# Kernel optimization log

Hardware: AMD Instinct MI355X
Metric: run time of the kernel (lower is better)

## Reference

```python
import jax, jax.numpy as jnp
import numpy as np


def setup_inputs() -> dict:
    key = jax.random.key(0)
    k1, k2, k3 = jax.random.split(key, 3)
    B, S, D_IN, D_OUT = 8, 512, 4096, 16384
    x = jax.random.normal(k1, (B, S, D_IN), dtype=jnp.float32)
    # int8 weights stored as int32 values in [-128, 127] (int8 semantics)
    weight_int8 = jax.random.randint(k2, (D_OUT, D_IN), -128, 128, dtype=jnp.int32)
    # per-tensor scale, e.g. max_abs/127 of an fp32 weight with std ~0.02
    weight_scale = jnp.float32(0.02 * 4.0 / 127.0)
    bias = jax.random.normal(k3, (D_OUT,), dtype=jnp.float32) * 0.01
    return {"x": x, "weight_int8": weight_int8, "weight_scale": weight_scale, "bias": bias}


def reference(x, weight_int8, weight_scale, bias):
    # dequantize: materialize fp32 weight (per-tensor scale, zero_point = 0)
    weight_fp32 = weight_int8.astype(jnp.float32) * weight_scale  # [O, I]
    # F.linear: y = x @ W^T + b
    out = jnp.einsum("bsi,oi->bso", x, weight_fp32) + bias
    return out
```

## Files before the change

### kernel.cpp

```cpp
#include <hip/hip_runtime.h>
#include <stdint.h>
#include <stddef.h>

typedef __attribute__((ext_vector_type(4))) int       i32x4;
typedef __attribute__((ext_vector_type(8))) short     bf16x8;
typedef __attribute__((ext_vector_type(4))) float     f32x4;
typedef __attribute__((ext_vector_type(4))) float     f32x4v;
typedef __attribute__((ext_vector_type(4))) unsigned short u16x4;

__device__ __forceinline__ unsigned short f2bf(float f) {
    union { float f; unsigned u; } v; v.f = f;
    unsigned r = v.u + 0x7FFFu + ((v.u >> 16) & 1u);
    return (unsigned short)(r >> 16);
}

__device__ __forceinline__ void gload_lds16(const void* g, void* l) {
    __builtin_amdgcn_global_load_lds(
        (const __attribute__((address_space(1))) void*)(g),
        (__attribute__((address_space(3))) void*)(l), 16, 0, 0);
}

__device__ __forceinline__ int pack4(float a, float b, float c, float d, float inv) {
    int r0 = ((int)rintf(a * inv)) & 255;
    int r1 = ((int)rintf(b * inv)) & 255;
    int r2 = ((int)rintf(c * inv)) & 255;
    int r3 = ((int)rintf(d * inv)) & 255;
    return r0 | (r1 << 8) | (r2 << 16) | (r3 << 24);
}

__global__ void cvt_x_q8(const float* __restrict__ x, signed char* __restrict__ xq,
                         float* __restrict__ sx, int K) {
    const int row = blockIdx.x;
    const int t   = threadIdx.x;
    const float* xr = x + (size_t)row * K;
    const int ng = K / 1024;

    f32x4v v[8];
    float am = 0.f;
#pragma unroll
    for (int i = 0; i < 8; ++i) {
        if (i < ng) {
            v[i] = ((const f32x4v*)xr)[i * 256 + t];
            am = fmaxf(am, fmaxf(fmaxf(fabsf(v[i][0]), fabsf(v[i][1])),
                                 fmaxf(fabsf(v[i][2]), fabsf(v[i][3]))));
        }
    }
#pragma unroll
    for (int m = 32; m >= 1; m >>= 1) am = fmaxf(am, __shfl_xor(am, m, 64));
    __shared__ float red[4];
    const int w = t >> 6;
    if ((t & 63) == 0) red[w] = am;
    __syncthreads();
    am = fmaxf(fmaxf(red[0], red[1]), fmaxf(red[2], red[3]));

    const float inv = (am > 0.f) ? 127.0f / am : 0.f;
    if (t == 0) sx[row] = (am > 0.f) ? am / 127.0f : 0.f;

    int* oq = (int*)(xq + (size_t)row * K);
#pragma unroll
    for (int i = 0; i < 8; ++i)
        if (i < ng) oq[i * 256 + t] = pack4(v[i][0], v[i][1], v[i][2], v[i][3], inv);
}

__global__ void cvt_w_q8(const int* __restrict__ w, signed char* __restrict__ o, int n4) {
    int i = blockIdx.x * blockDim.x + threadIdx.x;
    int stride = gridDim.x * blockDim.x;
    for (; i < n4; i += stride) {
        i32x4 a = ((const i32x4*)w)[i];
        ((int*)o)[i] = (a[0] & 255) | ((a[1] & 255) << 8) | ((a[2] & 255) << 16) | ((a[3] & 255) << 24);
    }
}

#define BM8 256
#define BN8 256
#define BKQ 128

__global__ __launch_bounds__(512, 2) void gemm8p_i8(
    const signed char* __restrict__ A,
    const signed char* __restrict__ Bw,
    const float* __restrict__ sx,
    const float* __restrict__ scale_p,
    const float* __restrict__ bias,
    float* __restrict__ C,
    int M, int N, int K)
{
    __shared__ __align__(16) char smem[131072];

    const int t    = threadIdx.x;
    const int lane = t & 63;
    const int w    = t >> 6;
    const int wm   = w >> 2;
    const int wn   = w & 3;

    int nwg = gridDim.x, bid = blockIdx.x;
    int swz = ((nwg & 7) == 0) ? ((bid & 7) * (nwg >> 3) + (bid >> 3)) : bid;
    const int ntn  = N / BN8;
    const int row0 = (swz / ntn) * BM8;
    const int col0 = (swz % ntn) * BN8;

    const int Kb = K;
    const int NT = K / BKQ;

    const int srow = w * 8 + (lane >> 3);
    const int sc2  = ((lane & 7) ^ (lane >> 3)) * 16;
    const int ldsLaneOff = w * 1024 + lane * 16;

    const char* aG = (const char*)A + (size_t)(row0 + srow) * Kb + sc2;
    const char* bG = (const char*)Bw + (size_t)(col0 + srow) * Kb + sc2;

    const int q    = lane >> 4;
    const int lr   = lane & 15;
    const int swzr = (lr & 7) << 4;

    i32x4 acc[8][4] = {};
    i32x4 aF[4][2], aS[4][2], bF[2][2], bS[2][2];

#define STG(gbase, h, tj, buf, region) do {                                   \
    const char* _g = (gbase) + (size_t)(h) * 128 * Kb + (size_t)(tj) * 128;   \
    char* _l = &smem[(buf) * 65536 + (region) * 16384 + ldsLaneOff];          \
    gload_lds16(_g, _l);                                                      \
    gload_lds16(_g + (size_t)64 * Kb, _l + 8192);                             \
} while (0)

#define RDA(buf, mi, ks) \
    (*(const i32x4*)&smem[(buf) * 65536 + wm * 16384 + ((mi) * 16 + lr) * 128 \
                          + ((((ks) << 6) | (q << 4)) ^ swzr)])
#define RDB(buf, nj, ks) \
    (*(const i32x4*)&smem[(buf) * 65536 + (2 + (wn >> 1)) * 16384              \
                          + ((wn & 1) * 64 + (nj) * 16 + lr) * 128             \
                          + ((((ks) << 6) | (q << 4)) ^ swzr)])

#define MFMA_(a, b, c) (c) = __builtin_amdgcn_mfma_i32_16x16x64_i8((a), (b), (c), 0, 0, 0)
#define BAR() __builtin_amdgcn_s_barrier()
#define LGKM0() do { asm volatile("s_waitcnt lgkmcnt(0)" ::: "memory"); \
                     __builtin_amdgcn_sched_barrier(0); } while (0)
#define VM4() asm volatile("s_waitcnt vmcnt(4)" ::: "memory")
#define VM0() asm volatile("s_waitcnt vmcnt(0)" ::: "memory")
#define VMNONE() do { } while (0)

#define TILE_STEP(tt, bb, stB, stA2, VMW) do {                                        \
                         \
    _Pragma("unroll") for (int mi = 0; mi < 4; ++mi) {                                \
        aF[mi][0] = RDA(bb, mi, 0); aF[mi][1] = RDA(bb, mi, 1); }                     \
    _Pragma("unroll") for (int nj = 0; nj < 2; ++nj) {                                \
        bF[nj][0] = RDB(bb, nj, 0); bF[nj][1] = RDB(bb, nj, 1); }                     \
    if (stB) STG(bG, 0, (tt) + 1, (bb) ^ 1, 2);                                       \
    BAR(); LGKM0();                                                                   \
    __builtin_amdgcn_s_setprio(1);                                                    \
    _Pragma("unroll") for (int mi = 0; mi < 4; ++mi)                                  \
    _Pragma("unroll") for (int nj = 0; nj < 2; ++nj) {                                \
        MFMA_(aF[mi][0], bF[nj][0], acc[mi][nj]);                                     \
        MFMA_(aF[mi][1], bF[nj][1], acc[mi][nj]); }                                   \
    __builtin_amdgcn_s_setprio(0);                                                    \
    BAR();                                                                            \
                               \
    _Pragma("unroll") for (int nj = 0; nj < 2; ++nj) {                                \
        bS[nj][0] = RDB(bb, 2 + nj, 0); bS[nj][1] = RDB(bb, 2 + nj, 1); }             \
    if (stB) STG(bG, 1, (tt) + 1, (bb) ^ 1, 3);                                       \
    BAR(); LGKM0();                                                                   \
    __builtin_amdgcn_s_setprio(1);                                                    \
    _Pragma("unroll") for (int mi = 0; mi < 4; ++mi)                                  \
    _Pragma("unroll") for (int nj = 0; nj < 2; ++nj) {                                \
        MFMA_(aF[mi][0], bS[nj][0], acc[mi][2 + nj]);                                 \
        MFMA_(aF[mi][1], bS[nj][1], acc[mi][2 + nj]); }                               \
    __builtin_amdgcn_s_setprio(0);                                                    \
    BAR();                                                                            \
                               \
    _Pragma("unroll") for (int mi = 0; mi < 4; ++mi) {                                \
        aS[mi][0] = RDA(bb, 4 + mi, 0); aS[mi][1] = RDA(bb, 4 + mi, 1); }             \
    if (stA2) STG(aG, 0, (tt) + 2, (bb), 0);                                          \
    BAR(); LGKM0();                                                                   \
    __builtin_amdgcn_s_setprio(1);                                                    \
    _Pragma("unroll") for (int mi = 0; mi < 4; ++mi)                                  \
    _Pragma("unroll") for (int nj = 0; nj < 2; ++nj) {                                \
        MFMA_(aS[mi][0], bS[nj][0], acc[4 + mi][2 + nj]);                             \
        MFMA_(aS[mi][1], bS[nj][1], acc[4 + mi][2 + nj]); }                           \
    __builtin_amdgcn_s_setprio(0);                                                    \
    BAR();                                                                            \
                \
    _Pragma("unroll") for (int nj = 0; nj < 2; ++nj) {                                \
        bF[nj][0] = RDB(bb, nj, 0); bF[nj][1] = RDB(bb, nj, 1); }                     \
    if (stA2) STG(aG, 1, (tt) + 2, (bb), 1);                                          \
    BAR(); LGKM0();                                                                   \
    __builtin_amdgcn_s_setprio(1);                                                    \
    _Pragma("unroll") for (int mi = 0; mi < 4; ++mi)                                  \
    _Pragma("unroll") for (int nj = 0; nj < 2; ++nj) {                                \
        MFMA_(aS[mi][0], bF[nj][0], acc[4 + mi][nj]);                                 \
        MFMA_(aS[mi][1], bF[nj][1], acc[4 + mi][nj]); }                               \
    __builtin_amdgcn_s_setprio(0);                                                    \
    VMW();                                                                            \
    BAR();                                                                            \
} while (0)

    STG(aG, 0, 0, 0, 0); STG(aG, 1, 0, 0, 1);
    STG(bG, 0, 0, 0, 2); STG(bG, 1, 0, 0, 3);
    STG(aG, 0, 1, 1, 0); STG(aG, 1, 1, 1, 1);
    VM4();
    BAR();

    for (int tt = 0; tt < NT - 2; tt += 2) {
        TILE_STEP(tt,     0, 1, 1, VM4);
        TILE_STEP(tt + 1, 1, 1, 1, VM4);
    }
    TILE_STEP(NT - 2, 0, 1, 0, VM0);
    TILE_STEP(NT - 1, 1, 0, 0, VMNONE);

    const float s = scale_p[0];
    float bv[4];
#pragma unroll
    for (int nj = 0; nj < 4; ++nj) bv[nj] = bias[col0 + wn * 64 + nj * 16 + lr];
#pragma unroll
    for (int mi = 0; mi < 8; ++mi) {
        const int rbase = row0 + wm * 128 + mi * 16 + q * 4;
        float sxr[4];
#pragma unroll
        for (int j = 0; j < 4; ++j) sxr[j] = sx[rbase + j] * s;
#pragma unroll
        for (int nj = 0; nj < 4; ++nj) {
            const int col = col0 + wn * 64 + nj * 16 + lr;
#pragma unroll
            for (int j = 0; j < 4; ++j)
                C[(size_t)(rbase + j) * N + col] = (float)acc[mi][nj][j] * sxr[j] + bv[nj];
        }
    }
#undef STG
#undef RDA
#undef RDB
#undef TILE_STEP
}

#define BM 128
#define BN 128
#define BK 64

__global__ __launch_bounds__(256, 2) void gemm_fused(
    const float* __restrict__ A,
    const int* __restrict__ Bw,
    const float* __restrict__ scale_p,
    const float* __restrict__ bias,
    float* __restrict__ C,
    int M, int N, int K)
{
    __shared__ unsigned short As[BM * BK];
    __shared__ unsigned short Bs[BN * BK];
    const int t = threadIdx.x, lane = t & 63, w = t >> 6;
    const int wm = w >> 1, wn = w & 1;
    int nwg = gridDim.x, bid = blockIdx.x;
    int swz = (nwg % 8 == 0) ? ((bid & 7) * (nwg >> 3) + (bid >> 3)) : bid;
    const int ntn = N / BN;
    const int row0 = (swz / ntn) * BM, col0 = (swz % ntn) * BN;
    f32x4 acc[4][4] = {};
    const int lr = lane & 15, lkbase = (lane >> 4) * 8;

    for (int kt = 0; kt < K; kt += BK) {
#pragma unroll
        for (int i = 0; i < 8; ++i) {
            const int r = i * 16 + (t >> 4), c = (t & 15) * 4;
            f32x4v v = *(const f32x4v*)&A[(size_t)(row0 + r) * K + kt + c];
            u16x4 o; o[0] = f2bf(v[0]); o[1] = f2bf(v[1]); o[2] = f2bf(v[2]); o[3] = f2bf(v[3]);
            *(u16x4*)&As[r * BK + c] = o;
        }
#pragma unroll
        for (int i = 0; i < 8; ++i) {
            const int r = i * 16 + (t >> 4), c = (t & 15) * 4;
            i32x4 v = *(const i32x4*)&Bw[(size_t)(col0 + r) * K + kt + c];
            u16x4 o; o[0] = f2bf((float)v[0]); o[1] = f2bf((float)v[1]);
                     o[2] = f2bf((float)v[2]); o[3] = f2bf((float)v[3]);
            *(u16x4*)&Bs[r * BK + c] = o;
        }
        __syncthreads();
#pragma unroll
        for (int ks = 0; ks < 2; ++ks) {
            const int lk = lkbase + ks * 32;
            bf16x8 af[4], bfr[4];
#pragma unroll
            for (int m = 0; m < 4; ++m) af[m] = *(const bf16x8*)&As[(wm * 64 + m * 16 + lr) * BK + lk];
#pragma unroll
            for (int n = 0; n < 4; ++n) bfr[n] = *(const bf16x8*)&Bs[(wn * 64 + n * 16 + lr) * BK + lk];
#pragma unroll
            for (int m = 0; m < 4; ++m)
#pragma unroll
                for (int n = 0; n < 4; ++n)
                    acc[m][n] = __builtin_amdgcn_mfma_f32_16x16x32_bf16(af[m], bfr[n], acc[m][n], 0, 0, 0);
        }
        __syncthreads();
    }
    const float s = scale_p[0];
    const int lq4 = (lane >> 4) * 4;
#pragma unroll
    for (int m = 0; m < 4; ++m)
#pragma unroll
        for (int n = 0; n < 4; ++n) {
            const int col = col0 + wn * 64 + n * 16 + lr;
            const float bv = bias[col];
#pragma unroll
            for (int j = 0; j < 4; ++j) {
                const int row = row0 + wm * 64 + m * 16 + lq4 + j;
                C[(size_t)row * N + col] = acc[m][n][j] * s + bv;
            }
        }
}

extern "C" void kernel_launch(void* const* d_in, const int* in_sizes, int n_in,
                              void* d_out, int out_size, void* d_ws, size_t ws_size,
                              hipStream_t stream) {
    const float* x     = (const float*)d_in[0];
    const int*   w8    = (const int*)d_in[1];
    const float* scale = (const float*)d_in[2];
    const float* bias  = (const float*)d_in[3];
    float* out = (float*)d_out;

    const int N = in_sizes[3];
    const int K = (int)((long)in_sizes[1] / N);
    const int M = (int)((long)in_sizes[0] / K);

    const size_t needA = (size_t)M * K;
    const size_t needB = (size_t)N * K;
    const size_t needS = (size_t)M * sizeof(float);
    const int NT = K / BKQ;

    const bool okShape = (M % BM8 == 0) && (N % BN8 == 0) && (K % BKQ == 0) &&
                         (K % 1024 == 0) && (K / 1024 <= 8) &&
                         (NT >= 4) && ((NT & 1) == 0);

    if (okShape && ws_size >= needA + needB + needS) {
        signed char* Aq = (signed char*)d_ws;
        signed char* Bq = Aq + needA;
        float*       sx = (float*)(Bq + needB);
        cvt_x_q8<<<M, 256, 0, stream>>>(x, Aq, sx, K);
        cvt_w_q8<<<4096, 256, 0, stream>>>(w8, Bq, (int)((size_t)N * K / 4));
        const int nblocks = (M / BM8) * (N / BN8);
        gemm8p_i8<<<nblocks, 512, 0, stream>>>(Aq, Bq, sx, scale, bias, out, M, N, K);
    } else {
        const int nblocks = (M / BM) * (N / BN);
        gemm_fused<<<nblocks, 256, 0, stream>>>(x, w8, scale, bias, out, M, N, K);
    }
}
```

Measured before the change: 358.3 us.

## Drop per-phase barriers in int8 GEMM loop and add nontemporal memory ops

Removes most workgroup barriers and explicit lgkmcnt waits inside each K-tile step of the int8 MFMA GEMM. Only two barriers per step remain, and they are paired with compiler fences. Both A-tile stagings for tile t+2 are merged into the last phase, after the barrier that ends all reads of that buffer. Nontemporal loads are added to the x and weight conversion kernels, and the GEMM epilogue uses nontemporal stores. The aim is to cut barrier stalls and let MFMA overlap with LDS reads, at the risk of subtle LDS race conditions if any ordering was relied on. The bf16 fallback kernel only gets a cosmetic index rewrite.

```diff
diff --git a/kernel.cpp b/kernel.cpp
--- a/kernel.cpp
+++ b/kernel.cpp
@@ -40,7 +40,7 @@
 #pragma unroll
     for (int i = 0; i < 8; ++i) {
         if (i < ng) {
-            v[i] = ((const f32x4v*)xr)[i * 256 + t];
+            v[i] = __builtin_nontemporal_load(&((const f32x4v*)xr)[i * 256 + t]);
             am = fmaxf(am, fmaxf(fmaxf(fabsf(v[i][0]), fabsf(v[i][1])),
                                  fmaxf(fabsf(v[i][2]), fabsf(v[i][3]))));
         }
@@ -66,7 +66,7 @@
     int i = blockIdx.x * blockDim.x + threadIdx.x;
     int stride = gridDim.x * blockDim.x;
     for (; i < n4; i += stride) {
-        i32x4 a = ((const i32x4*)w)[i];
+        i32x4 a = __builtin_nontemporal_load(&((const i32x4*)w)[i]);
         ((int*)o)[i] = (a[0] & 255) | ((a[1] & 255) << 8) | ((a[2] & 255) << 16) | ((a[3] & 255) << 24);
     }
 }
@@ -132,56 +132,48 @@
 
 #define MFMA_(a, b, c) (c) = __builtin_amdgcn_mfma_i32_16x16x64_i8((a), (b), (c), 0, 0, 0)
 #define BAR() __builtin_amdgcn_s_barrier()
-#define LGKM0() do { asm volatile("s_waitcnt lgkmcnt(0)" ::: "memory"); \
-                     __builtin_amdgcn_sched_barrier(0); } while (0)
+#define FENCE() asm volatile("" ::: "memory")
 #define VM4() asm volatile("s_waitcnt vmcnt(4)" ::: "memory")
 #define VM0() asm volatile("s_waitcnt vmcnt(0)" ::: "memory")
 #define VMNONE() do { } while (0)
 
 #define TILE_STEP(tt, bb, stB, stA2, VMW) do {                                        \
-                         \
+                              \
     _Pragma("unroll") for (int mi = 0; mi < 4; ++mi) {                                \
         aF[mi][0] = RDA(bb, mi, 0); aF[mi][1] = RDA(bb, mi, 1); }                     \
     _Pragma("unroll") for (int nj = 0; nj < 2; ++nj) {                                \
         bF[nj][0] = RDB(bb, nj, 0); bF[nj][1] = RDB(bb, nj, 1); }                     \
     if (stB) STG(bG, 0, (tt) + 1, (bb) ^ 1, 2);                                       \
-    BAR(); LGKM0();                                                                   \
     __builtin_amdgcn_s_setprio(1);                                                    \
     _Pragma("unroll") for (int mi = 0; mi < 4; ++mi)                                  \
     _Pragma("unroll") for (int nj = 0; nj < 2; ++nj) {                                \
         MFMA_(aF[mi][0], bF[nj][0], acc[mi][nj]);                                     \
         MFMA_(aF[mi][1], bF[nj][1], acc[mi][nj]); }                                   \
     __builtin_amdgcn_s_setprio(0);                                                    \
-    BAR();                                                                            \
-                               \
+                                 \
     _Pragma("unroll") for (int nj = 0; nj < 2; ++nj) {                                \
         bS[nj][0] = RDB(bb, 2 + nj, 0); bS[nj][1] = RDB(bb, 2 + nj, 1); }             \
     if (stB) STG(bG, 1, (tt) + 1, (bb) ^ 1, 3);                                       \
-    BAR(); LGKM0();                                                                   \
     __builtin_amdgcn_s_setprio(1);                                                    \
     _Pragma("unroll") for (int mi = 0; mi < 4; ++mi)                                  \
     _Pragma("unroll") for (int nj = 0; nj < 2; ++nj) {                                \
         MFMA_(aF[mi][0], bS[nj][0], acc[mi][2 + nj]);                                 \
         MFMA_(aF[mi][1], bS[nj][1], acc[mi][2 + nj]); }                               \
     __builtin_amdgcn_s_setprio(0);                                                    \
-    BAR();                                                                            \
-                               \
+                                                \
     _Pragma("unroll") for (int mi = 0; mi < 4; ++mi) {                                \
         aS[mi][0] = RDA(bb, 4 + mi, 0); aS[mi][1] = RDA(bb, 4 + mi, 1); }             \
-    if (stA2) STG(aG, 0, (tt) + 2, (bb), 0);                                          \
-    BAR(); LGKM0();                                                                   \
     __builtin_amdgcn_s_setprio(1);                                                    \
     _Pragma("unroll") for (int mi = 0; mi < 4; ++mi)                                  \
     _Pragma("unroll") for (int nj = 0; nj < 2; ++nj) {                                \
         MFMA_(aS[mi][0], bS[nj][0], acc[4 + mi][2 + nj]);                             \
         MFMA_(aS[mi][1], bS[nj][1], acc[4 + mi][2 + nj]); }                           \
     __builtin_amdgcn_s_setprio(0);                                                    \
-    BAR();                                                                            \
-                \
+    BAR(); FENCE();              \
+              \
     _Pragma("unroll") for (int nj = 0; nj < 2; ++nj) {                                \
         bF[nj][0] = RDB(bb, nj, 0); bF[nj][1] = RDB(bb, nj, 1); }                     \
-    if (stA2) STG(aG, 1, (tt) + 2, (bb), 1);                                          \
-    BAR(); LGKM0();                                                                   \
+    if (stA2) { STG(aG, 0, (tt) + 2, (bb), 0); STG(aG, 1, (tt) + 2, (bb), 1); }       \
     __builtin_amdgcn_s_setprio(1);                                                    \
     _Pragma("unroll") for (int mi = 0; mi < 4; ++mi)                                  \
     _Pragma("unroll") for (int nj = 0; nj < 2; ++nj) {                                \
@@ -189,14 +181,14 @@
         MFMA_(aS[mi][1], bF[nj][1], acc[4 + mi][nj]); }                               \
     __builtin_amdgcn_s_setprio(0);                                                    \
     VMW();                                                                            \
-    BAR();                                                                            \
+    BAR(); FENCE();              \
 } while (0)
 
     STG(aG, 0, 0, 0, 0); STG(aG, 1, 0, 0, 1);
     STG(bG, 0, 0, 0, 2); STG(bG, 1, 0, 0, 3);
     STG(aG, 0, 1, 1, 0); STG(aG, 1, 1, 1, 1);
     VM4();
-    BAR();
+    BAR(); FENCE();
 
     for (int tt = 0; tt < NT - 2; tt += 2) {
         TILE_STEP(tt,     0, 1, 1, VM4);
@@ -220,7 +212,8 @@
             const int col = col0 + wn * 64 + nj * 16 + lr;
 #pragma unroll
             for (int j = 0; j < 4; ++j)
-                C[(size_t)(rbase + j) * N + col] = (float)acc[mi][nj][j] * sxr[j] + bv[nj];
+                __builtin_nontemporal_store((float)acc[mi][nj][j] * sxr[j] + bv[nj],
+                                            &C[(size_t)(rbase + j) * N + col]);
         }
     }
 #undef STG
@@ -271,17 +264,18 @@
         __syncthreads();
 #pragma unroll
         for (int ks = 0; ks < 2; ++ks) {
-            const int lk = lkbase + ks * 32;
+            const int lk = lkbase + ks * 8 * 4;
             bf16x8 af[4], bfr[4];
 #pragma unroll
-            for (int m = 0; m < 4; ++m) af[m] = *(const bf16x8*)&As[(wm * 64 + m * 16 + lr) * BK + lk];
-#pragma unroll
-            for (int n = 0; n < 4; ++n) bfr[n] = *(const bf16x8*)&Bs[(wn * 64 + n * 16 + lr) * BK + lk];
+            for (int m = 0; m < 4; ++m) af[m] = *(const bf16x8*)&As[(wm * 64 + m * 16 + lr) * BK + lkbase + ks * 32];
+#pragma unroll
+            for (int n = 0; n < 4; ++n) bfr[n] = *(const bf16x8*)&Bs[(wn * 64 + n * 16 + lr) * BK + lkbase + ks * 32];
 #pragma unroll
             for (int m = 0; m < 4; ++m)
 #pragma unroll
                 for (int n = 0; n < 4; ++n)
                     acc[m][n] = __builtin_amdgcn_mfma_f32_16x16x32_bf16(af[m], bfr[n], acc[m][n], 0, 0, 0);
+            (void)lk;
         }
         __syncthreads();
     }
```

After: 341.1 us. -4.8%, faster.
